# Performance work log

Hardware: AMD Instinct MI355X
Metric: run time of the kernel (lower is better)

The kernel has to match this reference:

```python
import jax, jax.numpy as jnp
import numpy as np
import math

B, N, D, H, HC = 2, 2048, 1024, 16, 8
HIDDEN = 4 * D
MAX_PERIOD = 10000.0


def _timestep_embedding(t, dim):
    half = dim // 2
    freqs = jnp.exp(-math.log(MAX_PERIOD) * jnp.arange(half, dtype=jnp.float32) / half)
    args = t[:, None] * freqs[None, :]
    return jnp.concatenate([jnp.cos(args), jnp.sin(args)], axis=-1)


def _layer_norm(x, scale, bias, eps=1e-6):
    mu = jnp.mean(x, axis=-1, keepdims=True)
    var = jnp.mean(jnp.square(x - mu), axis=-1, keepdims=True)
    return (x - mu) * jax.lax.rsqrt(var + eps) * scale + bias


def _modulate(x, shift, scale):
    return x * (1.0 + scale[:, None, :]) + shift[:, None, :]


def setup_inputs():
    key = jax.random.key(0)
    ks = jax.random.split(key, 16)

    def dense(k, fin, fout):
        return jax.random.normal(k, (fin, fout), dtype=jnp.float32) / np.sqrt(fin)

    return {
        'x': jax.random.normal(ks[0], (B, N, D), dtype=jnp.float32),
        't': jax.random.uniform(ks[1], (B,), dtype=jnp.float32) * 1000.0,
        'norm1_scale': jnp.ones((D,), jnp.float32),
        'norm1_bias': jnp.zeros((D,), jnp.float32),
        'norm2_scale': jnp.ones((D,), jnp.float32),
        'norm2_bias': jnp.zeros((D,), jnp.float32),
        'tc_w1': dense(ks[2], HIDDEN, HIDDEN),
        'tc_b1': jnp.zeros((HIDDEN,), jnp.float32),
        'tc_w2': dense(ks[3], HIDDEN, HIDDEN),
        'tc_b2': jnp.zeros((HIDDEN,), jnp.float32),
        'tc_wa': 0.02 * dense(ks[4], HIDDEN, 4 * D),
        'tc_ba': jnp.zeros((4 * D,), jnp.float32),
        'tc_wc': 0.02 * dense(ks[5], HIDDEN, 4 * D),
        'tc_bc': jnp.zeros((4 * D,), jnp.float32),
        'attn_qk_w': dense(ks[6], D, D),
        'attn_v_w': dense(ks[7], D, D),
        'attn_out_w': dense(ks[8], D, D),
        'doob_w': 0.02 * dense(ks[9], D, 1),
        'doob_b': jnp.zeros((1,), jnp.float32),
        'ch_qk_w': dense(ks[10], D, D),
        'ch_v_w': dense(ks[11], D, D),
        'ch_out_w': dense(ks[12], D, D),
        'tau': jnp.ones((HC, 1, 1), jnp.float32),
        'gamma1': 1e-4 * jnp.ones((D,), jnp.float32),
        'gamma2': 1e-4 * jnp.ones((D,), jnp.float32),
    }


def reference(x, t, norm1_scale, norm1_bias, norm2_scale, norm2_bias,
              tc_w1, tc_b1, tc_w2, tc_b2, tc_wa, tc_ba, tc_wc, tc_bc,
              attn_qk_w, attn_v_w, attn_out_w, doob_w, doob_b,
              ch_qk_w, ch_v_w, ch_out_w, tau, gamma1, gamma2):
    # ---- AdaLN time conditioning ----
    emb = _timestep_embedding(t, HIDDEN)                 # (B, HIDDEN)
    h = jax.nn.silu(emb @ tc_w1 + tc_b1)
    h = jax.nn.silu(h @ tc_w2 + tc_b2)
    a_shift, a_scale, a_gate, a_lg = jnp.split(h @ tc_wa + tc_ba, 4, axis=-1)
    c_shift, c_scale, c_gate, c_lg = jnp.split(h @ tc_wc + tc_bc, 4, axis=-1)

    # ---- token-diffusion attention (MHDM, tied Q=K, Doob tilt) ----
    x1 = _modulate(_layer_norm(x, norm1_scale, norm1_bias), a_shift, a_scale)
    qk = (x1 @ attn_qk_w) * jnp.exp(a_lg)[:, None, :]    # (B,N,D)
    v = x1 @ attn_v_w
    dh = D // H
    qh = qk.reshape(B, N, H, dh).transpose(0, 2, 1, 3)   # (B,H,N,dh)
    vh = v.reshape(B, N, H, dh).transpose(0, 2, 1, 3)
    dot = jnp.einsum('bhmd,bhnd->bhmn', qh, qh)
    q2 = jnp.sum(qh * qh, axis=-1)
    logits = 2.0 * dot - q2[:, :, :, None] - q2[:, :, None, :]
    phi = (x1 @ doob_w + doob_b)[..., 0]                 # (B,N) destination tilt
    logits = logits + phi[:, None, None, :]
    attn = jax.nn.softmax(logits, axis=-1)
    w = jnp.einsum('bhmn,bhnd->bhmd', attn, vh)
    attn_out = w.transpose(0, 2, 1, 3).reshape(B, N, D) @ attn_out_w
    x = x + attn_out * a_gate[:, None, :] * gamma1

    # ---- channel-diffusion attention ----
    x2 = _modulate(_layer_norm(x, norm2_scale, norm2_bias), c_shift, c_scale)
    qkc = (x2 @ ch_qk_w) * jnp.exp(c_lg)[:, None, :]
    vc = x2 @ ch_v_w
    dhc = D // HC
    qkc = qkc.transpose(0, 2, 1).reshape(B, HC, dhc, N)  # (B,HC,dhc,N)
    vc = vc.transpose(0, 2, 1).reshape(B, HC, dhc, N)
    dotc = jnp.einsum('bhcn,bhdn->bhcd', qkc, qkc)
    q2c = jnp.sum(qkc * qkc, axis=-1)                    # (B,HC,dhc)
    logitsc = (2.0 * dotc - q2c[:, :, :, None] - q2c[:, :, None, :]) / math.sqrt(N)
    logitsc = logitsc * tau[None, ...]
    attnc = jax.nn.softmax(logitsc, axis=-1)
    wc = jnp.einsum('bhcd,bhdn->bhcn', attnc, vc)
    ch_out = wc.reshape(B, D, N).transpose(0, 2, 1) @ ch_out_w
    x = x + ch_out * c_gate[:, None, :] * gamma2
    return x
```

## Files before the change

kernel.cpp:

```cpp
#include <hip/hip_runtime.h>
#include <hip/hip_bf16.h>
#include <math.h>

typedef __bf16 bf16;
typedef bf16 bf16x8 __attribute__((ext_vector_type(8)));
typedef bf16 bf16x2 __attribute__((ext_vector_type(2)));
typedef float f32x4 __attribute__((ext_vector_type(4)));

#define B_   2
#define N_   2048
#define D_   1024
#define H_   16
#define HC_  8
#define M_   (B_*N_)

__device__ __forceinline__ void gl16(const bf16* g, bf16* lds_base) {
#if __has_builtin(__builtin_amdgcn_global_load_lds)
  __builtin_amdgcn_global_load_lds((const __attribute__((address_space(1))) void*)g,
                                   (__attribute__((address_space(3))) void*)lds_base,
                                   16, 0, 0);
#else
  int lane = threadIdx.x & 63;
  *(uint4*)(lds_base + lane * 8) = *(const uint4*)g;
#endif
}

__device__ __forceinline__ bf16x2 cvt_pk_bf16(float lo, float hi) {
  unsigned int r;
  asm("v_cvt_pk_bf16_f32 %0, %1, %2" : "=v"(r) : "v"(lo), "v"(hi));
  union { unsigned int u; bf16x2 v; } c;
  c.u = r;
  return c.v;
}

__global__ __launch_bounds__(256) void emb_kernel(const float* __restrict__ tin,
                                                  float* __restrict__ emb) {
  int idx = blockIdx.x * 256 + threadIdx.x;
  int b = idx >> 12, p = idx & 4095;
  float tv = tin[b];
  int half = p & 2047;
  float freq = expf(-logf(10000.f) * (float)half * (1.f / 2048.f));
  float arg = tv * freq;
  emb[idx] = (p < 2048) ? cosf(arg) : sinf(arg);
}

__global__ __launch_bounds__(256) void gemv_kernel(const float* __restrict__ x,
                                                   const float* __restrict__ W,
                                                   float* __restrict__ part) {
  __shared__ float xs[2][128];
  int t = threadIdx.x;
  int j0 = blockIdx.x * 512;
  int k0 = blockIdx.y * 128;
  if (t < 128) xs[0][t] = x[k0 + t];
  else         xs[1][t - 128] = x[4096 + k0 + (t - 128)];
  __syncthreads();
  float a00 = 0.f, a01 = 0.f, a10 = 0.f, a11 = 0.f;
  int j = j0 + t * 2;
  #pragma unroll 8
  for (int k = 0; k < 128; k++) {
    float2 wv = *(const float2*)(W + (size_t)(k0 + k) * 4096 + j);
    float x0 = xs[0][k], x1 = xs[1][k];
    a00 += x0 * wv.x; a01 += x0 * wv.y;
    a10 += x1 * wv.x; a11 += x1 * wv.y;
  }
  *(float2*)(part + (size_t)(blockIdx.y * 2 + 0) * 4096 + j) = make_float2(a00, a01);
  *(float2*)(part + (size_t)(blockIdx.y * 2 + 1) * 4096 + j) = make_float2(a10, a11);
}

__global__ __launch_bounds__(256) void gemv_reduce_kernel(const float* __restrict__ part,
                                                          const float* __restrict__ bias,
                                                          float* __restrict__ y, int act) {
  int idx = blockIdx.x * 256 + threadIdx.x;
  int b = idx >> 12, j = idx & 4095;
  float s = bias[j];
  #pragma unroll
  for (int kc = 0; kc < 32; kc++) s += part[(size_t)(kc * 2 + b) * 4096 + j];
  if (act) s = s / (1.f + expf(-s));
  y[idx] = s;
}

__global__ __launch_bounds__(256) void postA_kernel(const float* __restrict__ avec,
                                                    const float* __restrict__ cvec,
                                                    const float* __restrict__ g1,
                                                    const float* __restrict__ g2,
                                                    float* __restrict__ sca, float* __restrict__ scc,
                                                    float* __restrict__ agv, float* __restrict__ cgv) {
  int idx = blockIdx.x * 256 + threadIdx.x;
  int b = idx >> 10, d = idx & 1023;
  sca[idx] = expf(avec[b * 4096 + 3072 + d]);
  scc[idx] = expf(cvec[b * 4096 + 3072 + d]);
  agv[idx] = avec[b * 4096 + 2048 + d] * g1[d];
  cgv[idx] = cvec[b * 4096 + 2048 + d] * g2[d];
}

__global__ __launch_bounds__(256) void wtconv6_kernel(const float* w0, const float* w1,
                                                      const float* w2, const float* w3,
                                                      const float* w4, const float* w5,
                                                      bf16* o0, bf16* o1, bf16* o2,
                                                      bf16* o3, bf16* o4, bf16* o5) {
  const float* W; bf16* Wt;
  switch (blockIdx.z) {
    case 0: W = w0; Wt = o0; break;
    case 1: W = w1; Wt = o1; break;
    case 2: W = w2; Wt = o2; break;
    case 3: W = w3; Wt = o3; break;
    case 4: W = w4; Wt = o4; break;
    default: W = w5; Wt = o5; break;
  }
  __shared__ float tile[32][33];
  int t = threadIdx.x;
  int i = t >> 5, j = t & 31;
  int n0 = blockIdx.x * 32, k0 = blockIdx.y * 32;
  #pragma unroll
  for (int u = 0; u < 4; u++) {
    int k = i + u * 8;
    tile[k][j] = W[(size_t)(k0 + k) * 1024 + n0 + j];
  }
  __syncthreads();
  #pragma unroll
  for (int u = 0; u < 4; u++) {
    int n = i + u * 8;
    Wt[(size_t)(n0 + n) * 1024 + k0 + j] = (bf16)tile[j][n];
  }
}

__global__ __launch_bounds__(256) void ln_mod_kernel(const float* __restrict__ xin,
                                                     const float* __restrict__ nsc,
                                                     const float* __restrict__ nbi,
                                                     const float* __restrict__ mod,
                                                     const float* __restrict__ doobw,
                                                     float* __restrict__ phi,
                                                     bf16* __restrict__ outp) {
  int row = blockIdx.x;
  int b = row >> 11;
  int t = threadIdx.x;
  const float* xr = xin + (size_t)row * 1024;
  float v[4], s = 0.f, ss = 0.f;
  #pragma unroll
  for (int u = 0; u < 4; u++) { v[u] = xr[t + u * 256]; s += v[u]; ss += v[u] * v[u]; }
  #pragma unroll
  for (int off = 1; off < 64; off <<= 1) { s += __shfl_xor(s, off, 64); ss += __shfl_xor(ss, off, 64); }
  __shared__ float sb[4], ssb[4], pb[4];
  if ((t & 63) == 0) { sb[t >> 6] = s; ssb[t >> 6] = ss; }
  __syncthreads();
  s = sb[0] + sb[1] + sb[2] + sb[3];
  ss = ssb[0] + ssb[1] + ssb[2] + ssb[3];
  float mu = s * (1.f / 1024.f);
  float var = ss * (1.f / 1024.f) - mu * mu;
  float rs = rsqrtf(var + 1e-6f);
  const float* shv = mod + b * 4096;
  const float* scv = mod + b * 4096 + 1024;
  float ph = 0.f;
  #pragma unroll
  for (int u = 0; u < 4; u++) {
    int d = t + u * 256;
    float y = (v[u] - mu) * rs * nsc[d] + nbi[d];
    float ym = y * (1.f + scv[d]) + shv[d];
    outp[(size_t)row * 1024 + d] = (bf16)ym;
    if (doobw) ph += ym * doobw[d];
  }
  if (doobw) {
    #pragma unroll
    for (int off = 1; off < 64; off <<= 1) ph += __shfl_xor(ph, off, 64);
    if ((t & 63) == 0) pb[t >> 6] = ph;
    __syncthreads();
    if (t == 0) phi[row] = pb[0] + pb[1] + pb[2] + pb[3];
  }
}

__global__ __launch_bounds__(256) void phimax_kernel(const float* __restrict__ phi,
                                                     float* __restrict__ pm) {
  int b = blockIdx.x;
  int t = threadIdx.x;
  float m = -1e30f;
  #pragma unroll
  for (int u = 0; u < 8; u++) m = fmaxf(m, phi[b * 2048 + t + u * 256]);
  #pragma unroll
  for (int off = 1; off < 64; off <<= 1) m = fmaxf(m, __shfl_xor(m, off, 64));
  __shared__ float mb[4];
  if ((t & 63) == 0) mb[t >> 6] = m;
  __syncthreads();
  if (t == 0) pm[b] = fmaxf(fmaxf(mb[0], mb[1]), fmaxf(mb[2], mb[3]));
}

template <int MODE, int TM>
__global__ __launch_bounds__(256) void gemm_kernel(const bf16* __restrict__ A,
                                                   const bf16* __restrict__ Wt,
                                                   const float* __restrict__ scale,
                                                   const float* __restrict__ resid,
                                                   void* __restrict__ out0,
                                                   void* __restrict__ out1) {
  constexpr int K = 1024;
  constexpr int WM = TM / 2;
  constexpr int IT = WM / 16;
  __shared__ bf16 As[TM * 64];
  __shared__ bf16 Bs[128 * 64];
  const int m0 = blockIdx.x * TM;
  const int n0 = blockIdx.y * 128;
  const int t = threadIdx.x, lane = t & 63, wid = t >> 6;
  const int wy = wid >> 1, wx = wid & 1;
  const int ml = lane & 15, quad = lane >> 4, rq = quad * 4, kq = quad * 8;
  const int srow = lane >> 3;
  const int schunk = (lane & 7) ^ srow;
  const bf16* gA = A  + (size_t)(m0 + wid * (TM / 4) + srow) * K + schunk * 8;
  const bf16* gB = Wt + (size_t)(n0 + wid * 32 + srow) * K + schunk * 8;
  bf16* lA = As + (wid * (TM / 4)) * 64;
  bf16* lB = Bs + (wid * 32) * 64;
  const int mlm = ml & 7;

  f32x4 acc[IT][4] = {};
  for (int k0 = 0; k0 < K; k0 += 64) {
    __syncthreads();
    #pragma unroll
    for (int q = 0; q < TM / 32; q++)
      gl16(gA + (size_t)q * 8 * K + k0, lA + q * 8 * 64);
    #pragma unroll
    for (int q = 0; q < 4; q++)
      gl16(gB + (size_t)q * 8 * K + k0, lB + q * 8 * 64);
    __syncthreads();
    #pragma unroll
    for (int ks = 0; ks < 2; ks++) {
      const int slot = ((ks * 4 + quad) ^ mlm) * 8;
      bf16x8 af[IT], bfv[4];
      #pragma unroll
      for (int i = 0; i < IT; i++)
        af[i] = *(const bf16x8*)(As + (wy * WM + i * 16 + ml) * 64 + slot);
      #pragma unroll
      for (int j = 0; j < 4; j++)
        bfv[j] = *(const bf16x8*)(Bs + (wx * 64 + j * 16 + ml) * 64 + slot);
      #pragma unroll
      for (int i = 0; i < IT; i++)
        #pragma unroll
        for (int j = 0; j < 4; j++)
          acc[i][j] = __builtin_amdgcn_mfma_f32_16x16x32_bf16(af[i], bfv[j], acc[i][j], 0, 0, 0);
    }
  }
  #pragma unroll
  for (int i = 0; i < IT; i++) {
    #pragma unroll
    for (int j = 0; j < 4; j++) {
      int col = n0 + wx * 64 + j * 16 + ml;
      #pragma unroll
      for (int r = 0; r < 4; r++) {
        int row = m0 + wy * WM + i * 16 + rq + r;
        int b = row >> 11, n = row & 2047;
        float val = acc[i][j][r];
        if constexpr (MODE == 10) {
          if (col < 1024) {
            int h = col >> 6, dh = col & 63;
            ((bf16*)out0)[((size_t)(b * 16 + h) * 2048 + n) * 64 + dh] =
                (bf16)(val * scale[b * 1024 + col]);
          } else {
            int c2 = col - 1024;
            int h = c2 >> 6, dh = c2 & 63;
            ((bf16*)out1)[(((size_t)(b * 16 + h) * 32 + (n >> 6)) * 64 + dh) * 64 + (n & 63)] =
                (bf16)val;
          }
        } else if constexpr (MODE == 11) {
          if (col < 1024) {
            float sv = val * scale[b * 1024 + col];
            ((bf16*)out0)[((size_t)((b * 8 + (col >> 7)) * 128 + (col & 127))) * 2048 + n] = (bf16)sv;
          } else {
            ((bf16*)out1)[(size_t)row * 1024 + (col - 1024)] = (bf16)val;
          }
        } else {
          float g = scale[b * 1024 + col];
          ((float*)out0)[(size_t)row * 1024 + col] =
              resid[(size_t)row * 1024 + col] + val * g;
        }
      }
    }
  }
}

__global__ __launch_bounds__(256) void q2e_kernel(const bf16* __restrict__ qkh,
                                                  const float* __restrict__ phi,
                                                  const float* __restrict__ pm,
                                                  float* __restrict__ q2buf,
                                                  float* __restrict__ ebuf) {
  int idx = blockIdx.x * 256 + threadIdx.x;
  int bh = idx >> 11, n = idx & 2047;
  int b = bh >> 4;
  const bf16* qr = qkh + (size_t)idx * 64;
  float q = 0.f;
  #pragma unroll
  for (int u = 0; u < 8; u++) {
    bf16x8 v = *(const bf16x8*)(qr + u * 8);
    #pragma unroll
    for (int e = 0; e < 8; e++) { float f = (float)v[e]; q += f * f; }
  }
  q2buf[idx] = q * 1.44269504f;
  ebuf[idx]  = (phi[b * 2048 + n] - q - pm[b]) * 1.44269504f;
}

__global__ __launch_bounds__(256, 4) void flash_kernel(const bf16* __restrict__ qkh,
                                                       const bf16* __restrict__ vtb,
                                                       const float* __restrict__ q2buf,
                                                       const float* __restrict__ ebuf,
                                                       bf16* __restrict__ wout) {
  int bid = blockIdx.x;
  int ii = bid >> 3;
  int bh = (bid & 7) * 4 + (ii >> 5);
  int mt = ii & 31;
  int b = bh >> 4, h = bh & 15;
  int m0 = mt * 64;
  int t = threadIdx.x, lane = t & 63, w = t >> 6;
  int ml = lane & 15, quad = lane >> 4;
  int mlm = ml & 7, q1 = quad & 1, qh = quad >> 1;

  __shared__ __align__(16) bf16 Ks[2][64 * 64];
  __shared__ __align__(16) bf16 Vs[2][64 * 64];
  __shared__ __align__(16) bf16 Ps[4 * 16 * 64];

  int sr = lane >> 3, swz = (lane & 7) ^ sr;
  const bf16* gK = qkh + ((size_t)bh * 2048 + w * 16 + sr) * 64 + swz * 8;
  const bf16* gV = vtb + (size_t)bh * 131072 + (w * 16 + sr) * 64 + swz * 8;

  const bf16* qrow = qkh + ((size_t)bh * 2048 + m0 + w * 16 + ml) * 64;
  bf16x8 qf0 = *(const bf16x8*)(qrow + quad * 8);
  bf16x8 qf1 = *(const bf16x8*)(qrow + 32 + quad * 8);

  float q2l = q2buf[(size_t)bh * 2048 + m0 + w * 16 + ml];
  const float* ep = ebuf + (size_t)bh * 2048;

  bf16* Pb = Ps + (w * 16 + ml) * 64;
  f32x4 oacc[4] = {};
  float rs = 0.f;

  gl16(gK,       &Ks[0][w * 1024]);
  gl16(gK + 512, &Ks[0][w * 1024 + 512]);
  gl16(gV,       &Vs[0][w * 1024]);
  gl16(gV + 512, &Vs[0][w * 1024 + 512]);

  #pragma unroll 2
  for (int nc = 0; nc < 32; nc++) {
    int cur = nc & 1;
    __syncthreads();
    if (nc + 1 < 32) {
      const bf16* nk = gK + (size_t)(nc + 1) * 4096;
      const bf16* nv = gV + (size_t)(nc + 1) * 4096;
      bf16* dk = &Ks[cur ^ 1][w * 1024];
      bf16* dv = &Vs[cur ^ 1][w * 1024];
      gl16(nk,       dk);
      gl16(nk + 512, dk + 512);
      gl16(nv,       dv);
      gl16(nv + 512, dv + 512);
    }
    const bf16* Kc = Ks[cur];
    const bf16* Vc = Vs[cur];

    f32x4 sacc[4] = {};
    __builtin_amdgcn_s_setprio(1);
    #pragma unroll
    for (int ks = 0; ks < 2; ks++) {
      bf16x8 qb = ks ? qf1 : qf0;
      #pragma unroll
      for (int j = 0; j < 4; j++) {
        bf16x8 ka = *(const bf16x8*)(Kc + (j * 16 + ml) * 64 + ((4 * ks + quad) ^ mlm) * 8);
        sacc[j] = __builtin_amdgcn_mfma_f32_16x16x32_bf16(ka, qb, sacc[j], 0, 0, 0);
      }
    }
    __builtin_amdgcn_s_setprio(0);

    const float* epc = ep + nc * 64;
    #pragma unroll
    for (int j = 0; j < 4; j++) {
      float4 ev = *(const float4*)(epc + j * 16 + quad * 4);
      float p0 = exp2f(fmaf(2.88539008f, sacc[j][0], ev.x - q2l));
      float p1 = exp2f(fmaf(2.88539008f, sacc[j][1], ev.y - q2l));
      float p2 = exp2f(fmaf(2.88539008f, sacc[j][2], ev.z - q2l));
      float p3 = exp2f(fmaf(2.88539008f, sacc[j][3], ev.w - q2l));
      rs += (p0 + p1) + (p2 + p3);
      int sl = (((2 * j + qh) ^ mlm) * 4 + 2 * q1) * 2;
      *(bf16x2*)(Pb + sl)     = cvt_pk_bf16(p0, p1);
      *(bf16x2*)(Pb + sl + 2) = cvt_pk_bf16(p2, p3);
    }
    __builtin_amdgcn_sched_barrier(0);

    __builtin_amdgcn_s_setprio(1);
    #pragma unroll
    for (int ks = 0; ks < 2; ks++) {
      bf16x8 pa = *(const bf16x8*)(Pb + ((4 * ks + quad) ^ mlm) * 8);
      #pragma unroll
      for (int jd = 0; jd < 4; jd++) {
        bf16x8 vb = *(const bf16x8*)(Vc + (jd * 16 + ml) * 64 + ((4 * ks + quad) ^ mlm) * 8);
        oacc[jd] = __builtin_amdgcn_mfma_f32_16x16x32_bf16(pa, vb, oacc[jd], 0, 0, 0);
      }
    }
    __builtin_amdgcn_s_setprio(0);
  }

  rs += __shfl_xor(rs, 16, 64);
  rs += __shfl_xor(rs, 32, 64);
  float rinv = 1.f / rs;

  int rq = quad * 4;
  float rv[4];
  #pragma unroll
  for (int r = 0; r < 4; r++) rv[r] = __shfl(rinv, rq + r, 64);

  bf16* wrow = wout + (size_t)(b * 2048 + m0 + w * 16) * 1024 + h * 64;
  #pragma unroll
  for (int jd = 0; jd < 4; jd++)
    #pragma unroll
    for (int r = 0; r < 4; r++)
      wrow[(size_t)(rq + r) * 1024 + jd * 16 + ml] = (bf16)(oacc[jd][r] * rv[r]);
}

__global__ __launch_bounds__(256) void gram_kernel(const bf16* __restrict__ qkct,
                                                   float* __restrict__ dotp) {
  int bh = blockIdx.x, ksl = blockIdx.y;
  const bf16* Q = qkct + (size_t)bh * 128 * 2048 + ksl * 256;
  __shared__ bf16 Ts[128 * 40];
  int t = threadIdx.x, lane = t & 63, w = t >> 6;
  int ml = lane & 15, kq = (lane >> 4) * 8, rq = (lane >> 4) * 4;
  f32x4 acc[2][8] = {};
  for (int k0 = 0; k0 < 256; k0 += 32) {
    __syncthreads();
    #pragma unroll
    for (int u = 0; u < 2; u++) {
      int idx = u * 256 + t;
      int r = idx >> 2, seg = (idx & 3) * 8;
      *(uint4*)(Ts + r * 40 + seg) = *(const uint4*)(Q + (size_t)r * 2048 + k0 + seg);
    }
    __syncthreads();
    bf16x8 afr[2], bfr[8];
    #pragma unroll
    for (int i = 0; i < 2; i++) afr[i] = *(const bf16x8*)(Ts + (w * 32 + i * 16 + ml) * 40 + kq);
    #pragma unroll
    for (int j = 0; j < 8; j++) bfr[j] = *(const bf16x8*)(Ts + (j * 16 + ml) * 40 + kq);
    #pragma unroll
    for (int i = 0; i < 2; i++)
      #pragma unroll
      for (int j = 0; j < 8; j++)
        acc[i][j] = __builtin_amdgcn_mfma_f32_16x16x32_bf16(afr[i], bfr[j], acc[i][j], 0, 0, 0);
  }
  float* outp = dotp + ((size_t)ksl * 16 + bh) * 16384;
  #pragma unroll
  for (int i = 0; i < 2; i++)
    #pragma unroll
    for (int j = 0; j < 8; j++)
      #pragma unroll
      for (int r = 0; r < 4; r++) {
        int c = w * 32 + i * 16 + rq + r, d = j * 16 + ml;
        outp[c * 128 + d] = acc[i][j][r];
      }
}

__global__ __launch_bounds__(128) void chsm_kernel(const float* __restrict__ dotp,
                                                   const float* __restrict__ tau,
                                                   bf16* __restrict__ attnc) {
  int blk = blockIdx.x;
  int bh = blk >> 7, c = blk & 127, hc = bh & 7;
  int d = threadIdx.x;
  float dot = 0.f, dd = 0.f;
  #pragma unroll
  for (int kc = 0; kc < 8; kc++) {
    const float* pp = dotp + ((size_t)kc * 16 + bh) * 16384;
    dot += pp[c * 128 + d];
    dd  += pp[d * 128 + d];
  }
  __shared__ float diag[128];
  __shared__ float red[2], red2[2];
  diag[d] = dd;
  __syncthreads();
  float qc = diag[c];
  float sc = tau[hc] * rsqrtf(2048.f);
  float lg = sc * (2.f * dot - qc - dd);
  float mx = lg;
  #pragma unroll
  for (int off = 1; off < 64; off <<= 1) mx = fmaxf(mx, __shfl_xor(mx, off, 64));
  if ((d & 63) == 0) red[d >> 6] = mx;
  __syncthreads();
  mx = fmaxf(red[0], red[1]);
  float e = exp2f((lg - mx) * 1.44269504f);
  float sm = e;
  #pragma unroll
  for (int off = 1; off < 64; off <<= 1) sm += __shfl_xor(sm, off, 64);
  if ((d & 63) == 0) red2[d >> 6] = sm;
  __syncthreads();
  sm = red2[0] + red2[1];
  attnc[(size_t)bh * 16384 + c * 128 + d] = (bf16)(e / sm);
}

__global__ __launch_bounds__(256) void chav_kernel(const bf16* __restrict__ attnc,
                                                   const bf16* __restrict__ vc,
                                                   bf16* __restrict__ wcn) {
  int nb = blockIdx.x, bh = blockIdx.y;
  int b = bh >> 3, hc = bh & 7;
  int n0 = nb * 64;
  __shared__ bf16 As[128 * 136];
  __shared__ bf16 Bs[64 * 136];
  int t = threadIdx.x, lane = t & 63, w = t >> 6;
  int ml = lane & 15, kq = (lane >> 4) * 8, rq = (lane >> 4) * 4;
  #pragma unroll
  for (int u = 0; u < 8; u++) {
    int idx = u * 256 + t;
    int r = idx >> 4, seg = (idx & 15) * 8;
    *(uint4*)(As + r * 136 + seg) = *(const uint4*)(attnc + (size_t)bh * 16384 + r * 128 + seg);
  }
  #pragma unroll
  for (int u = 0; u < 4; u++) {
    int idx = u * 256 + t;
    int r = idx >> 4, seg = (idx & 15) * 8;
    *(uint4*)(Bs + r * 136 + seg) =
        *(const uint4*)(vc + (size_t)(b * 2048 + n0 + r) * 1024 + hc * 128 + seg);
  }
  __syncthreads();
  f32x4 acc[2][4] = {};
  #pragma unroll
  for (int ks = 0; ks < 4; ks++) {
    bf16x8 afr[2], bfr[4];
    #pragma unroll
    for (int i = 0; i < 2; i++)
      afr[i] = *(const bf16x8*)(As + (w * 32 + i * 16 + ml) * 136 + ks * 32 + kq);
    #pragma unroll
    for (int j = 0; j < 4; j++)
      bfr[j] = *(const bf16x8*)(Bs + (j * 16 + ml) * 136 + ks * 32 + kq);
    #pragma unroll
    for (int i = 0; i < 2; i++)
      #pragma unroll
      for (int j = 0; j < 4; j++)
        acc[i][j] = __builtin_amdgcn_mfma_f32_16x16x32_bf16(afr[i], bfr[j], acc[i][j], 0, 0, 0);
  }
  #pragma unroll
  for (int i = 0; i < 2; i++)
    #pragma unroll
    for (int j = 0; j < 4; j++)
      #pragma unroll
      for (int r = 0; r < 4; r++) {
        int c = w * 32 + i * 16 + rq + r;
        int n = n0 + j * 16 + ml;
        wcn[(size_t)(b * 2048 + n) * 1024 + hc * 128 + c] = (bf16)acc[i][j][r];
      }
}

extern "C" void kernel_launch(void* const* d_in, const int* in_sizes, int n_in,
                              void* d_out, int out_size, void* d_ws, size_t ws_size,
                              hipStream_t stream) {
  const float* x      = (const float*)d_in[0];
  const float* t      = (const float*)d_in[1];
  const float* n1s    = (const float*)d_in[2];
  const float* n1b    = (const float*)d_in[3];
  const float* n2s    = (const float*)d_in[4];
  const float* n2b    = (const float*)d_in[5];
  const float* tc_w1  = (const float*)d_in[6];
  const float* tc_b1  = (const float*)d_in[7];
  const float* tc_w2  = (const float*)d_in[8];
  const float* tc_b2  = (const float*)d_in[9];
  const float* tc_wa  = (const float*)d_in[10];
  const float* tc_ba  = (const float*)d_in[11];
  const float* tc_wc  = (const float*)d_in[12];
  const float* tc_bc  = (const float*)d_in[13];
  const float* aqk_w  = (const float*)d_in[14];
  const float* av_w   = (const float*)d_in[15];
  const float* aout_w = (const float*)d_in[16];
  const float* doobw  = (const float*)d_in[17];
  const float* cqk_w  = (const float*)d_in[19];
  const float* cv_w   = (const float*)d_in[20];
  const float* cout_w = (const float*)d_in[21];
  const float* tau    = (const float*)d_in[22];
  const float* g1     = (const float*)d_in[23];
  const float* g2     = (const float*)d_in[24];
  float* out = (float*)d_out;

  char* p = (char*)d_ws;
  auto alloc = [&](size_t bytes) -> void* {
    void* r = (void*)p;
    p += (bytes + 255) & ~(size_t)255;
    return r;
  };
  float* emb   = (float*)alloc(2 * 4096 * 4);
  float* partA = (float*)alloc(32 * 2 * 4096 * 4);
  float* partB = (float*)alloc(32 * 2 * 4096 * 4);
  float* h1    = (float*)alloc(2 * 4096 * 4);
  float* h2    = (float*)alloc(2 * 4096 * 4);
  float* avec  = (float*)alloc(2 * 4096 * 4);
  float* cvec  = (float*)alloc(2 * 4096 * 4);
  float* sca   = (float*)alloc(2 * 1024 * 4);
  float* scc   = (float*)alloc(2 * 1024 * 4);
  float* agv   = (float*)alloc(2 * 1024 * 4);
  float* cgv   = (float*)alloc(2 * 1024 * 4);
  float* phi   = (float*)alloc(4096 * 4);
  float* pmax  = (float*)alloc(2 * 4);
  float* q2buf = (float*)alloc(2 * 16 * 2048 * 4);
  float* ebuf  = (float*)alloc(2 * 16 * 2048 * 4);
  float* dotp  = (float*)alloc((size_t)8 * 16 * 16384 * 4);
  bf16* attnc  = (bf16*)alloc(16 * 128 * 128 * 2);
  bf16* wt     = (bf16*)alloc((size_t)6 * 1024 * 1024 * 2);
  bf16* xbf    = (bf16*)alloc((size_t)M_ * 1024 * 2);
  bf16* qkbf   = (bf16*)alloc((size_t)M_ * 1024 * 2);
  bf16* vbuf   = (bf16*)alloc((size_t)M_ * 1024 * 2);
  bf16* wbuf   = (bf16*)alloc((size_t)M_ * 1024 * 2);
  (void)ws_size; (void)in_sizes; (void)n_in; (void)out_size;

  bf16* wt_tok  = wt;
  bf16* wt_out  = wt + (size_t)2 * 1048576;
  bf16* wt_ch   = wt + (size_t)3 * 1048576;
  bf16* wt_cout = wt + (size_t)5 * 1048576;

  dim3 blk(256);
  wtconv6_kernel<<<dim3(32, 32, 6), blk, 0, stream>>>(
      aqk_w, av_w, aout_w, cqk_w, cv_w, cout_w,
      wt_tok, wt_tok + (size_t)1048576, wt_out,
      wt_ch,  wt_ch  + (size_t)1048576, wt_cout);

  emb_kernel<<<32, blk, 0, stream>>>(t, emb);
  gemv_kernel<<<dim3(8, 32), blk, 0, stream>>>(emb, tc_w1, partA);
  gemv_reduce_kernel<<<32, blk, 0, stream>>>(partA, tc_b1, h1, 1);
  gemv_kernel<<<dim3(8, 32), blk, 0, stream>>>(h1, tc_w2, partA);
  gemv_reduce_kernel<<<32, blk, 0, stream>>>(partA, tc_b2, h2, 1);
  gemv_kernel<<<dim3(8, 32), blk, 0, stream>>>(h2, tc_wa, partA);
  gemv_kernel<<<dim3(8, 32), blk, 0, stream>>>(h2, tc_wc, partB);
  gemv_reduce_kernel<<<32, blk, 0, stream>>>(partA, tc_ba, avec, 0);
  gemv_reduce_kernel<<<32, blk, 0, stream>>>(partB, tc_bc, cvec, 0);
  postA_kernel<<<8, blk, 0, stream>>>(avec, cvec, g1, g2, sca, scc, agv, cgv);

  ln_mod_kernel<<<4096, blk, 0, stream>>>(x, n1s, n1b, avec, doobw, phi, xbf);
  phimax_kernel<<<2, blk, 0, stream>>>(phi, pmax);
  gemm_kernel<10, 128><<<dim3(32, 16), blk, 0, stream>>>(xbf, wt_tok, sca, nullptr, qkbf, vbuf);
  q2e_kernel<<<256, blk, 0, stream>>>(qkbf, phi, pmax, q2buf, ebuf);
  flash_kernel<<<dim3(1024), dim3(256), 0, stream>>>(qkbf, vbuf, q2buf, ebuf, wbuf);
  gemm_kernel<4, 64><<<dim3(64, 8), blk, 0, stream>>>(wbuf, wt_out, agv, x, out, nullptr);

  ln_mod_kernel<<<4096, blk, 0, stream>>>(out, n2s, n2b, cvec, nullptr, nullptr, xbf);
  gemm_kernel<11, 128><<<dim3(32, 16), blk, 0, stream>>>(xbf, wt_ch, scc, nullptr, qkbf, vbuf);
  gram_kernel<<<dim3(16, 8), blk, 0, stream>>>(qkbf, dotp);
  chsm_kernel<<<2048, dim3(128), 0, stream>>>(dotp, tau, attnc);
  chav_kernel<<<dim3(32, 16), blk, 0, stream>>>(attnc, vbuf, wbuf);
  gemm_kernel<4, 64><<<dim3(64, 8), blk, 0, stream>>>(wbuf, wt_cout, cgv, out, out, nullptr);
}
```

Measured before the change: 575.5 us.

## Keep flash P in registers via permuted V layout and stage tilt in LDS

Result: faster. 544.2 us (-5.4%).

```diff
diff --git a/kernel.cpp b/kernel.cpp
--- a/kernel.cpp
+++ b/kernel.cpp
@@ -4,6 +4,7 @@
 
 typedef __bf16 bf16;
 typedef bf16 bf16x8 __attribute__((ext_vector_type(8)));
+typedef bf16 bf16x4 __attribute__((ext_vector_type(4)));
 typedef bf16 bf16x2 __attribute__((ext_vector_type(2)));
 typedef float f32x4 __attribute__((ext_vector_type(4)));
 
@@ -25,12 +26,27 @@
 #endif
 }
 
+__device__ __forceinline__ void gl4(const float* g, float* lds_base) {
+#if __has_builtin(__builtin_amdgcn_global_load_lds)
+  __builtin_amdgcn_global_load_lds((const __attribute__((address_space(1))) void*)g,
+                                   (__attribute__((address_space(3))) void*)lds_base,
+                                   4, 0, 0);
+#else
+  int lane = threadIdx.x & 63;
+  lds_base[lane] = *g;
+#endif
+}
+
 __device__ __forceinline__ bf16x2 cvt_pk_bf16(float lo, float hi) {
   unsigned int r;
   asm("v_cvt_pk_bf16_f32 %0, %1, %2" : "=v"(r) : "v"(lo), "v"(hi));
   union { unsigned int u; bf16x2 v; } c;
   c.u = r;
   return c.v;
+}
+
+__device__ __forceinline__ int vperm(int kv) {
+  return (((kv >> 4) & 1) << 5) | (((kv >> 2) & 3) << 3) | (((kv >> 5) & 1) << 2) | (kv & 3);
 }
 
 __global__ __launch_bounds__(256) void emb_kernel(const float* __restrict__ tin,
@@ -240,34 +256,45 @@
     #pragma unroll
     for (int j = 0; j < 4; j++) {
       int col = n0 + wx * 64 + j * 16 + ml;
-      #pragma unroll
-      for (int r = 0; r < 4; r++) {
-        int row = m0 + wy * WM + i * 16 + rq + r;
-        int b = row >> 11, n = row & 2047;
-        float val = acc[i][j][r];
-        if constexpr (MODE == 10) {
-          if (col < 1024) {
-            int h = col >> 6, dh = col & 63;
-            ((bf16*)out0)[((size_t)(b * 16 + h) * 2048 + n) * 64 + dh] =
-                (bf16)(val * scale[b * 1024 + col]);
-          } else {
-            int c2 = col - 1024;
-            int h = c2 >> 6, dh = c2 & 63;
-            ((bf16*)out1)[(((size_t)(b * 16 + h) * 32 + (n >> 6)) * 64 + dh) * 64 + (n & 63)] =
-                (bf16)val;
-          }
-        } else if constexpr (MODE == 11) {
-          if (col < 1024) {
-            float sv = val * scale[b * 1024 + col];
-            ((bf16*)out0)[((size_t)((b * 8 + (col >> 7)) * 128 + (col & 127))) * 2048 + n] = (bf16)sv;
-          } else {
-            ((bf16*)out1)[(size_t)row * 1024 + (col - 1024)] = (bf16)val;
-          }
+      int row0 = m0 + wy * WM + i * 16 + rq;
+      int b0 = row0 >> 11, nn0 = row0 & 2047;
+      if constexpr (MODE == 10) {
+        if (col < 1024) {
+          int h = col >> 6, dh = col & 63;
+          float sv = scale[b0 * 1024 + col];
+          #pragma unroll
+          for (int r = 0; r < 4; r++)
+            ((bf16*)out0)[((size_t)(b0 * 16 + h) * 2048 + nn0 + r) * 64 + dh] =
+                (bf16)(acc[i][j][r] * sv);
         } else {
-          float g = scale[b * 1024 + col];
-          ((float*)out0)[(size_t)row * 1024 + col] =
-              resid[(size_t)row * 1024 + col] + val * g;
+          int c2 = col - 1024;
+          int h = c2 >> 6, dh = c2 & 63;
+          int c = vperm(nn0 & 63);
+          union { bf16x4 v; bf16x2 h2[2]; } pk;
+          pk.h2[0] = cvt_pk_bf16(acc[i][j][0], acc[i][j][1]);
+          pk.h2[1] = cvt_pk_bf16(acc[i][j][2], acc[i][j][3]);
+          *(bf16x4*)((bf16*)out1 +
+              (((size_t)(b0 * 16 + h) * 32 + (nn0 >> 6)) * 64 + dh) * 64 + c) = pk.v;
         }
+      } else if constexpr (MODE == 11) {
+        if (col < 1024) {
+          float sv = scale[b0 * 1024 + col];
+          union { bf16x4 v; bf16x2 h2[2]; } pk;
+          pk.h2[0] = cvt_pk_bf16(acc[i][j][0] * sv, acc[i][j][1] * sv);
+          pk.h2[1] = cvt_pk_bf16(acc[i][j][2] * sv, acc[i][j][3] * sv);
+          *(bf16x4*)((bf16*)out0 +
+              ((size_t)((b0 * 8 + (col >> 7)) * 128 + (col & 127))) * 2048 + nn0) = pk.v;
+        } else {
+          #pragma unroll
+          for (int r = 0; r < 4; r++)
+            ((bf16*)out1)[(size_t)(row0 + r) * 1024 + (col - 1024)] = (bf16)acc[i][j][r];
+        }
+      } else {
+        float g = scale[b0 * 1024 + col];
+        #pragma unroll
+        for (int r = 0; r < 4; r++)
+          ((float*)out0)[(size_t)(row0 + r) * 1024 + col] =
+              resid[(size_t)(row0 + r) * 1024 + col] + acc[i][j][r] * g;
       }
     }
   }
@@ -306,24 +333,23 @@
   int m0 = mt * 64;
   int t = threadIdx.x, lane = t & 63, w = t >> 6;
   int ml = lane & 15, quad = lane >> 4;
-  int mlm = ml & 7, q1 = quad & 1, qh = quad >> 1;
+  int mlm = ml & 7;
 
   __shared__ __align__(16) bf16 Ks[2][64 * 64];
   __shared__ __align__(16) bf16 Vs[2][64 * 64];
-  __shared__ __align__(16) bf16 Ps[4 * 16 * 64];
+  __shared__ __align__(16) float Es[2][64];
 
   int sr = lane >> 3, swz = (lane & 7) ^ sr;
   const bf16* gK = qkh + ((size_t)bh * 2048 + w * 16 + sr) * 64 + swz * 8;
   const bf16* gV = vtb + (size_t)bh * 131072 + (w * 16 + sr) * 64 + swz * 8;
+  const float* ep = ebuf + (size_t)bh * 2048;
 
   const bf16* qrow = qkh + ((size_t)bh * 2048 + m0 + w * 16 + ml) * 64;
   bf16x8 qf0 = *(const bf16x8*)(qrow + quad * 8);
   bf16x8 qf1 = *(const bf16x8*)(qrow + 32 + quad * 8);
 
   float q2l = q2buf[(size_t)bh * 2048 + m0 + w * 16 + ml];
-  const float* ep = ebuf + (size_t)bh * 2048;
-
-  bf16* Pb = Ps + (w * 16 + ml) * 64;
+
   f32x4 oacc[4] = {};
   float rs = 0.f;
 
@@ -331,6 +357,7 @@
   gl16(gK + 512, &Ks[0][w * 1024 + 512]);
   gl16(gV,       &Vs[0][w * 1024]);
   gl16(gV + 512, &Vs[0][w * 1024 + 512]);
+  if (w == 0) gl4(ep + lane, Es[0]);
 
   #pragma unroll 2
   for (int nc = 0; nc < 32; nc++) {
@@ -345,6 +372,7 @@
       gl16(nk + 512, dk + 512);
       gl16(nv,       dv);
       gl16(nv + 512, dv + 512);
+      if (w == 0) gl4(ep + (nc + 1) * 64 + lane, Es[cur ^ 1]);
     }
     const bf16* Kc = Ks[cur];
     const bf16* Vc = Vs[cur];
@@ -362,25 +390,30 @@
     }
     __builtin_amdgcn_s_setprio(0);
 
-    const float* epc = ep + nc * 64;
+    float pv[4][4];
     #pragma unroll
     for (int j = 0; j < 4; j++) {
-      float4 ev = *(const float4*)(epc + j * 16 + quad * 4);
-      float p0 = exp2f(fmaf(2.88539008f, sacc[j][0], ev.x - q2l));
-      float p1 = exp2f(fmaf(2.88539008f, sacc[j][1], ev.y - q2l));
-      float p2 = exp2f(fmaf(2.88539008f, sacc[j][2], ev.z - q2l));
-      float p3 = exp2f(fmaf(2.88539008f, sacc[j][3], ev.w - q2l));
-      rs += (p0 + p1) + (p2 + p3);
-      int sl = (((2 * j + qh) ^ mlm) * 4 + 2 * q1) * 2;
-      *(bf16x2*)(Pb + sl)     = cvt_pk_bf16(p0, p1);
-      *(bf16x2*)(Pb + sl + 2) = cvt_pk_bf16(p2, p3);
+      float4 ev = *(const float4*)(&Es[cur][j * 16 + quad * 4]);
+      pv[j][0] = exp2f(fmaf(2.88539008f, sacc[j][0], ev.x - q2l));
+      pv[j][1] = exp2f(fmaf(2.88539008f, sacc[j][1], ev.y - q2l));
+      pv[j][2] = exp2f(fmaf(2.88539008f, sacc[j][2], ev.z - q2l));
+      pv[j][3] = exp2f(fmaf(2.88539008f, sacc[j][3], ev.w - q2l));
+      rs += (pv[j][0] + pv[j][1]) + (pv[j][2] + pv[j][3]);
     }
-    __builtin_amdgcn_sched_barrier(0);
+    union { bf16x8 v; bf16x2 h2[4]; } pa0, pa1;
+    pa0.h2[0] = cvt_pk_bf16(pv[0][0], pv[0][1]);
+    pa0.h2[1] = cvt_pk_bf16(pv[0][2], pv[0][3]);
+    pa0.h2[2] = cvt_pk_bf16(pv[2][0], pv[2][1]);
+    pa0.h2[3] = cvt_pk_bf16(pv[2][2], pv[2][3]);
+    pa1.h2[0] = cvt_pk_bf16(pv[1][0], pv[1][1]);
+    pa1.h2[1] = cvt_pk_bf16(pv[1][2], pv[1][3]);
+    pa1.h2[2] = cvt_pk_bf16(pv[3][0], pv[3][1]);
+    pa1.h2[3] = cvt_pk_bf16(pv[3][2], pv[3][3]);
 
     __builtin_amdgcn_s_setprio(1);
     #pragma unroll
     for (int ks = 0; ks < 2; ks++) {
-      bf16x8 pa = *(const bf16x8*)(Pb + ((4 * ks + quad) ^ mlm) * 8);
+      bf16x8 pa = ks ? pa1.v : pa0.v;
       #pragma unroll
       for (int jd = 0; jd < 4; jd++) {
         bf16x8 vb = *(const bf16x8*)(Vc + (jd * 16 + ml) * 64 + ((4 * ks + quad) ^ mlm) * 8);
```
